# Optimization experiments

Hardware: AMD Instinct MI355X
Metric: run time of the kernel (lower is better)

Reference implementation:

```python
import jax, jax.numpy as jnp
import numpy as np

B, L, D, H = 2, 2048, 2048, 16
HD = D // H  # 128, must be even for RoPE


def rope(x, seq_len, theta=10000.0):
    """Apply RoPE to x of shape [B, H, L, Dh]."""
    d = x.shape[-1]
    freqs = 1.0 / theta ** (jnp.arange(0, d, 2, dtype=x.dtype) / d)  # [d/2]
    t = jnp.arange(seq_len, dtype=x.dtype)
    f = jnp.outer(t, freqs)                      # [L, d/2]
    sin = jnp.repeat(jnp.sin(f), 2, axis=-1)     # [L, d]
    cos = jnp.repeat(jnp.cos(f), 2, axis=-1)
    x1, x2 = x[..., ::2], x[..., 1::2]
    x_rot = jnp.stack([-x2, x1], axis=-1).reshape(x.shape)
    return x * cos + x_rot * sin


def setup_inputs() -> dict:
    key = jax.random.key(0)
    k1, k2, k3 = jax.random.split(key, 3)
    x = jax.random.normal(k1, (B, L, D), dtype=jnp.float32)
    w_qkv = jax.random.normal(k2, (D, 3 * D), dtype=jnp.float32) * (1.0 / np.sqrt(D))
    w_proj = jax.random.normal(k3, (D, D), dtype=jnp.float32) * (1.0 / np.sqrt(D))
    return {"x": x, "w_qkv": w_qkv, "w_proj": w_proj}


def reference(x, w_qkv, w_proj):
    Bc, Lc, Dc = x.shape
    scale = 1.0 / np.sqrt(HD)
    qkv = (x @ w_qkv).reshape(Bc, Lc, 3, H, HD)
    q, k, v = qkv[:, :, 0], qkv[:, :, 1], qkv[:, :, 2]   # [B, L, H, Dh]
    # transpose to [B, H, L, Dh], then RoPE (position axis = L)
    q = rope(jnp.transpose(q, (0, 2, 1, 3)), Lc)
    k = rope(jnp.transpose(k, (0, 2, 1, 3)), Lc)
    v = jnp.transpose(v, (0, 2, 1, 3))
    att = jnp.einsum("bhqd,bhkd->bhqk", q, k) * scale   # [B, H, L, L]
    att = jax.nn.softmax(att, axis=-1)
    out = jnp.einsum("bhqk,bhkd->bhqd", att, v)          # [B, H, L, Dh]
    out = jnp.transpose(out, (0, 2, 1, 3)).reshape(Bc, Lc, Dc)
    return out @ w_proj
```

## Files before the change

kernel.cpp:

```cpp
#include <hip/hip_runtime.h>
#include <hip/hip_bf16.h>
#include <cstdint>

typedef short short8 __attribute__((ext_vector_type(8)));
typedef float f32x4 __attribute__((ext_vector_type(4)));

#define AS1 __attribute__((address_space(1)))
#define AS3 __attribute__((address_space(3)))

static __device__ __forceinline__ void async_cp16(const void* g, void* l) {
  __builtin_amdgcn_global_load_lds((const AS1 unsigned int*)g, (AS3 unsigned int*)l, 16, 0, 0);
}

static __device__ __forceinline__ ushort f2bf(float f) {
  unsigned u = __builtin_bit_cast(unsigned, f);
  u += 0x7fffu + ((u >> 16) & 1u);
  return (ushort)(u >> 16);
}
static __device__ __forceinline__ float bf2f(ushort h) {
  unsigned u = ((unsigned)h) << 16;
  return __builtin_bit_cast(float, u);
}

#define FENCE asm volatile("" ::: "memory")
#define BARRIER do { FENCE; __builtin_amdgcn_s_barrier(); FENCE; } while (0)
#define WAITLGKM asm volatile("s_waitcnt lgkmcnt(0)" ::: "memory")
#define WAITVM(N) asm volatile("s_waitcnt vmcnt(" #N ")" ::: "memory")

__global__ void cvt_bf16_kernel(const float* __restrict__ in, ushort* __restrict__ out, int n4) {
  int i = blockIdx.x * blockDim.x + threadIdx.x;
  if (i >= n4) return;
  float4 v = ((const float4*)in)[i];
  ushort4 o;
  o.x = f2bf(v.x); o.y = f2bf(v.y); o.z = f2bf(v.z); o.w = f2bf(v.w);
  ((ushort4*)out)[i] = o;
}

__global__ void transpose_cvt_kernel(const float* __restrict__ in, ushort* __restrict__ out,
                                     int R, int C) {
  __shared__ ushort tile[32][33];
  int c0 = blockIdx.x * 32, r0 = blockIdx.y * 32;
  int tx = threadIdx.x, ty = threadIdx.y;
  for (int j = 0; j < 32; j += 8)
    tile[ty + j][tx] = f2bf(in[(size_t)(r0 + ty + j) * C + c0 + tx]);
  __syncthreads();
  for (int j = 0; j < 32; j += 8)
    out[(size_t)(c0 + ty + j) * R + r0 + tx] = tile[tx][ty + j];
}

__global__ __launch_bounds__(512, 2) void gemm_qkv_kernel(
    const ushort* __restrict__ A, const ushort* __restrict__ Bt,
    ushort* __restrict__ qr, ushort* __restrict__ kr, ushort* __restrict__ vt,
    int K, int N) {
  __shared__ __align__(16) ushort smem[65536];
  const int tid = threadIdx.x;
  const int wave = tid >> 6, lane = tid & 63;
  const int wm = wave >> 2, wn = wave & 3;
  const int m0 = blockIdx.y * 256, n0 = blockIdx.x * 256;
  const int frl = lane & 15, fq = lane >> 4;
  const int sx = fq ^ (frl & 7);
  const int srow = tid >> 3;
  const int slog8 = (((tid & 7) ^ ((tid >> 3) & 7)) << 3);

  const ushort* aG = A + (size_t)(m0 + srow) * K + slog8;
  const ushort* bG = Bt + (size_t)(n0 + srow) * K + slog8;
  ushort* lw = smem + wave * 512;

  f32x4 acc[8][4] = {};
  short8 aF[4][2], bF[2][2][2];

  auto stA = [&](int tt, int h) {
    ushort* l = lw + (tt & 1) * 32768 + h * 8192;
    const ushort* g = aG + (size_t)(h * 128) * K + tt * 64;
    async_cp16(g, l);
    async_cp16(g + (size_t)64 * K, l + 4096);
  };
  auto stB = [&](int tt, int h) {
    ushort* l = lw + (tt & 1) * 32768 + 16384 + h * 8192;
    const ushort* g = bG + (size_t)(h * 128) * K + tt * 64;
    async_cp16(g, l);
    async_cp16(g + (size_t)64 * K, l + 4096);
  };
  auto LDA = [&](int buf, int mh) {
#pragma unroll
    for (int mf = 0; mf < 4; ++mf)
#pragma unroll
      for (int kk = 0; kk < 2; ++kk)
        aF[mf][kk] = *(const short8*)(smem + buf * 32768 +
            (wm * 128 + mh * 64 + mf * 16 + frl) * 64 + ((sx ^ (kk << 2)) << 3));
  };
  auto LDB = [&](int buf, int nh) {
#pragma unroll
    for (int j = 0; j < 2; ++j)
#pragma unroll
      for (int kk = 0; kk < 2; ++kk)
        bF[nh][j][kk] = *(const short8*)(smem + buf * 32768 + 16384 +
            (wn * 64 + nh * 32 + j * 16 + frl) * 64 + ((sx ^ (kk << 2)) << 3));
  };
  auto MFMAQ = [&](int mh, int nh) {
    __builtin_amdgcn_s_setprio(1);
#pragma unroll
    for (int mf = 0; mf < 4; ++mf)
#pragma unroll
      for (int j = 0; j < 2; ++j)
#pragma unroll
        for (int kk = 0; kk < 2; ++kk)
          acc[mh * 4 + mf][nh * 2 + j] = __builtin_amdgcn_mfma_f32_16x16x32_bf16(
              aF[mf][kk], bF[nh][j][kk], acc[mh * 4 + mf][nh * 2 + j], 0, 0, 0);
    __builtin_amdgcn_s_setprio(0);
  };

  stB(0, 0); stB(0, 1); stA(0, 0); stA(0, 1);
  stB(1, 0); stB(1, 1);
  WAITVM(4);
  BARRIER;

  const int NT = K >> 6;
  for (int i = 0; i < NT / 2 - 1; ++i) {
    const int t = 2 * i;
    LDA(0, 0); LDB(0, 0); stA(t + 1, 0);
    BARRIER; WAITLGKM; MFMAQ(0, 0); BARRIER;
    LDB(0, 1); stA(t + 1, 1);
    BARRIER; WAITLGKM; MFMAQ(0, 1); BARRIER;
    LDA(0, 1); stB(t + 2, 0);
    BARRIER; WAITLGKM; MFMAQ(1, 0); BARRIER;
    stB(t + 2, 1);
    BARRIER; WAITLGKM; MFMAQ(1, 1); WAITVM(4); BARRIER;
    LDA(1, 0); LDB(1, 0); stA(t + 2, 0);
    BARRIER; WAITLGKM; MFMAQ(0, 0); BARRIER;
    LDB(1, 1); stA(t + 2, 1);
    BARRIER; WAITLGKM; MFMAQ(0, 1); BARRIER;
    LDA(1, 1); stB(t + 3, 0);
    BARRIER; WAITLGKM; MFMAQ(1, 0); BARRIER;
    stB(t + 3, 1);
    BARRIER; WAITLGKM; MFMAQ(1, 1); WAITVM(4); BARRIER;
  }
  {
    const int t = NT - 2;
    LDA(0, 0); LDB(0, 0); stA(t + 1, 0);
    BARRIER; WAITLGKM; MFMAQ(0, 0); BARRIER;
    LDB(0, 1); stA(t + 1, 1);
    BARRIER; WAITLGKM; MFMAQ(0, 1); BARRIER;
    LDA(0, 1);
    BARRIER; WAITLGKM; MFMAQ(1, 0); BARRIER;
    BARRIER; WAITLGKM; MFMAQ(1, 1); WAITVM(0); BARRIER;
    LDA(1, 0); LDB(1, 0);
    BARRIER; WAITLGKM; MFMAQ(0, 0); BARRIER;
    LDB(1, 1);
    BARRIER; WAITLGKM; MFMAQ(0, 1); BARRIER;
    LDA(1, 1);
    BARRIER; WAITLGKM; MFMAQ(1, 0); BARRIER;
    BARRIER; WAITLGKM; MFMAQ(1, 1); BARRIER;
  }

  const int rq = fq * 4;
  if (n0 < 4096) {
    ushort* dst = (n0 >= 2048) ? kr : qr;
#pragma unroll
    for (int mi = 0; mi < 8; ++mi)
#pragma unroll
      for (int ni = 0; ni < 4; ++ni) {
        int col = n0 + wn * 64 + ni * 16 + frl;
        int rem = col & 2047, h = rem >> 7, dh = rem & 127;
#pragma unroll
        for (int r = 0; r < 4; ++r) {
          int row = m0 + wm * 128 + mi * 16 + rq + r;
          int b = row >> 11, l = row & 2047;
          dst[((size_t)((b << 4) + h) * 2048 + l) * 128 + dh] = f2bf(acc[mi][ni][r]);
        }
      }
  } else {
    ushort* vtile = smem + wave * 1024;
    const int col0 = n0 + wn * 64;
    const int row0 = m0 + wm * 128;
    const int b = row0 >> 11, l0 = row0 & 2047;
    const int swz = (frl & 3) << 4;
#pragma unroll
    for (int hm = 0; hm < 2; ++hm)
#pragma unroll
      for (int ni = 0; ni < 4; ++ni) {
#pragma unroll
        for (int mi = 0; mi < 4; ++mi)
#pragma unroll
          for (int r = 0; r < 4; ++r) {
            int ll = mi * 16 + rq + r;
            vtile[frl * 64 + (ll ^ swz)] = f2bf(acc[hm * 4 + mi][ni][r]);
          }
#pragma unroll
        for (int tt = 0; tt < 2; ++tt) {
          int dl = tt * 8 + (lane >> 3);
          int l8 = (lane & 7) * 8;
          int lsw = l8 ^ ((dl & 3) << 4);
          int rem = (col0 + ni * 16 + dl) & 2047;
          int h = rem >> 7, dh = rem & 127;
          *(short8*)(vt + ((size_t)((b << 4) + h) * 128 + dh) * 2048 + l0 + hm * 64 + l8) =
              *(const short8*)(vtile + dl * 64 + lsw);
        }
      }
  }
}

__global__ __launch_bounds__(256) void gemm_out_kernel(
    const ushort* __restrict__ A, const ushort* __restrict__ Bt,
    float* __restrict__ C, int K, int N) {
  __shared__ __align__(16) ushort As[128 * 32];
  __shared__ __align__(16) ushort Bs[128 * 32];
  const int tid = threadIdx.x;
  const int wave = tid >> 6, lane = tid & 63;
  const int wr = (wave >> 1) * 64, wc = (wave & 1) * 64;
  const int m0 = blockIdx.y * 128, n0 = blockIdx.x * 128;
  const int l4 = lane >> 2, lb8 = (lane & 3) * 8;
  const int fr = lane & 15, fq8 = (lane >> 4) * 8;

  f32x4 acc[4][4] = {};

  for (int k0 = 0; k0 < K; k0 += 32) {
#pragma unroll
    for (int j = 0; j < 2; ++j) {
      const int r = wave * 32 + j * 16 + l4;
      async_cp16(A + (size_t)(m0 + r) * K + k0 + lb8, As + wave * 1024 + j * 512);
      async_cp16(Bt + (size_t)(n0 + r) * K + k0 + lb8, Bs + wave * 1024 + j * 512);
    }
    __syncthreads();
    short8 af[4], bf_[4];
#pragma unroll
    for (int i = 0; i < 4; ++i) {
      af[i] = *(const short8*)(As + (wr + i * 16 + fr) * 32 + fq8);
      bf_[i] = *(const short8*)(Bs + (wc + i * 16 + fr) * 32 + fq8);
    }
#pragma unroll
    for (int mi = 0; mi < 4; ++mi)
#pragma unroll
      for (int ni = 0; ni < 4; ++ni)
        acc[mi][ni] = __builtin_amdgcn_mfma_f32_16x16x32_bf16(af[mi], bf_[ni], acc[mi][ni], 0, 0, 0);
    __syncthreads();
  }

  const int rq = (lane >> 4) * 4;
#pragma unroll
  for (int mi = 0; mi < 4; ++mi)
#pragma unroll
    for (int ni = 0; ni < 4; ++ni) {
      int col = n0 + wc + ni * 16 + fr;
#pragma unroll
      for (int r = 0; r < 4; ++r) {
        int row = m0 + wr + mi * 16 + rq + r;
        C[(size_t)row * N + col] = acc[mi][ni][r];
      }
    }
}

__global__ void rope_kernel(ushort* __restrict__ q, ushort* __restrict__ k) {
  int idx = blockIdx.x * 256 + threadIdx.x;
  int i = idx & 63;
  int l = (idx >> 6) & 2047;
  int bh = idx >> 17;
  float inv = __builtin_amdgcn_exp2f(-(float)i * (13.287712379549449f / 64.0f));
  float f = (float)l * inv;
  float s, c;
  sincosf(f, &s, &c);
  size_t base = ((size_t)bh * 2048 + l) * 128 + 2 * i;
  float q0 = bf2f(q[base]), q1 = bf2f(q[base + 1]);
  q[base] = f2bf(q0 * c - q1 * s);
  q[base + 1] = f2bf(q1 * c + q0 * s);
  float k0 = bf2f(k[base]), k1 = bf2f(k[base + 1]);
  k[base] = f2bf(k0 * c - k1 * s);
  k[base + 1] = f2bf(k1 * c + k0 * s);
}

__global__ __launch_bounds__(512, 4) void flash_kernel(
    const ushort* __restrict__ qr, const ushort* __restrict__ kr,
    const ushort* __restrict__ vtg, ushort* __restrict__ att) {
  __shared__ __align__(16) ushort Ks[64 * 136];
  __shared__ __align__(16) ushort Vt[128 * 68];
  __shared__ __align__(16) ushort Ps[8 * 16 * 68];

  const int tid = threadIdx.x;
  const int wave = tid >> 6, lane = tid & 63;
  const int bid = blockIdx.x;
  const int swzb = (bid & 7) * 64 + (bid >> 3);
  const int qt = swzb & 15;
  const int bh = swzb >> 4;
  const int q0 = qt * 128 + wave * 16;
  const size_t bh_base = (size_t)bh * 2048 * 128;

  const int fr = lane & 15;
  const int fq = lane >> 4;
  const float cs = 0.08838834764831845f * 1.4426950408889634f;

  short8 qf[4];
  {
    const ushort* qp = qr + bh_base + (size_t)(q0 + fr) * 128 + fq * 8;
#pragma unroll
    for (int kc = 0; kc < 4; ++kc) qf[kc] = *(const short8*)(qp + kc * 32);
  }

  f32x4 oacc[8];
#pragma unroll
  for (int i = 0; i < 8; ++i) oacc[i] = (f32x4){0.f, 0.f, 0.f, 0.f};
  float l_r[4] = {0.f, 0.f, 0.f, 0.f};

  const int krow = tid >> 3;
  const int kc8 = tid & 7;
  const int vrow = tid >> 2;
  const int vc8 = tid & 3;

  ushort* pw = &Ps[wave * 16 * 68];

  short8 kpre[2], vpre[2];
  {
    const ushort* kg = kr + bh_base + (size_t)krow * 128;
    const ushort* vg = vtg + bh_base + (size_t)vrow * 2048;
#pragma unroll
    for (int i = 0; i < 2; ++i) {
      kpre[i] = *(const short8*)(kg + (kc8 + 8 * i) * 8);
      vpre[i] = *(const short8*)(vg + (vc8 + 4 * i) * 8);
    }
  }

  for (int kt = 0; kt < 32; ++kt) {
    __syncthreads();
#pragma unroll
    for (int i = 0; i < 2; ++i) {
      *(short8*)(&Ks[krow * 136 + (kc8 + 8 * i) * 8]) = kpre[i];
      *(short8*)(&Vt[vrow * 68 + (vc8 + 4 * i) * 8]) = vpre[i];
    }
    __syncthreads();
    if (kt < 31) {
      const ushort* kg = kr + bh_base + (size_t)((kt + 1) * 64 + krow) * 128;
      const ushort* vg = vtg + bh_base + (size_t)vrow * 2048 + (kt + 1) * 64;
#pragma unroll
      for (int i = 0; i < 2; ++i) {
        kpre[i] = *(const short8*)(kg + (kc8 + 8 * i) * 8);
        vpre[i] = *(const short8*)(vg + (vc8 + 4 * i) * 8);
      }
    }

    float sv[4][4];
    __builtin_amdgcn_s_setprio(1);
#pragma unroll
    for (int nt = 0; nt < 4; ++nt) {
      f32x4 a = (f32x4){0.f, 0.f, 0.f, 0.f};
#pragma unroll
      for (int kc = 0; kc < 4; ++kc) {
        short8 kf = *(const short8*)(&Ks[(nt * 16 + fr) * 136 + kc * 32 + fq * 8]);
        a = __builtin_amdgcn_mfma_f32_16x16x32_bf16(qf[kc], kf, a, 0, 0, 0);
      }
#pragma unroll
      for (int r = 0; r < 4; ++r) sv[nt][r] = a[r];
    }
    __builtin_amdgcn_s_setprio(0);

#pragma unroll
    for (int nt = 0; nt < 4; ++nt)
#pragma unroll
      for (int r = 0; r < 4; ++r) {
        float pv = __builtin_amdgcn_exp2f(sv[nt][r] * cs);
        l_r[r] += pv;
        pw[(fq * 4 + r) * 68 + nt * 16 + fr] = f2bf(pv);
      }

    __builtin_amdgcn_s_setprio(1);
#pragma unroll
    for (int kc2 = 0; kc2 < 2; ++kc2) {
      short8 pf = *(const short8*)(&pw[fr * 68 + kc2 * 32 + fq * 8]);
#pragma unroll
      for (int dt = 0; dt < 8; ++dt) {
        short8 vf = *(const short8*)(&Vt[(dt * 16 + fr) * 68 + kc2 * 32 + fq * 8]);
        oacc[dt] = __builtin_amdgcn_mfma_f32_16x16x32_bf16(pf, vf, oacc[dt], 0, 0, 0);
      }
    }
    __builtin_amdgcn_s_setprio(0);
  }

  const int b = bh >> 4, h = bh & 15;
#pragma unroll
  for (int r = 0; r < 4; ++r) {
    float l = l_r[r];
    l += __shfl_xor(l, 1);
    l += __shfl_xor(l, 2);
    l += __shfl_xor(l, 4);
    l += __shfl_xor(l, 8);
    float inv = 1.0f / l;
    size_t row = (size_t)(b * 2048 + q0 + fq * 4 + r) * 2048 + h * 128;
#pragma unroll
    for (int dt = 0; dt < 8; ++dt)
      att[row + dt * 16 + fr] = f2bf(oacc[dt][r] * inv);
  }
}

extern "C" void kernel_launch(void* const* d_in, const int* in_sizes, int n_in,
                              void* d_out, int out_size, void* d_ws, size_t ws_size,
                              hipStream_t stream) {
  const float* x = (const float*)d_in[0];
  const float* w_qkv = (const float*)d_in[1];
  const float* w_proj = (const float*)d_in[2];
  float* out = (float*)d_out;

  char* p = (char*)d_ws;
  ushort* xb = (ushort*)p;  p += (size_t)4096 * 2048 * 2;
  ushort* wqt = (ushort*)p; p += (size_t)6144 * 2048 * 2;
  ushort* wpt = (ushort*)p; p += (size_t)2048 * 2048 * 2;
  ushort* qr = (ushort*)p;  p += (size_t)32 * 2048 * 128 * 2;
  ushort* kr = (ushort*)p;  p += (size_t)32 * 2048 * 128 * 2;
  ushort* vt = (ushort*)p;  p += (size_t)32 * 2048 * 128 * 2;
  ushort* att = (ushort*)p; p += (size_t)4096 * 2048 * 2;

  cvt_bf16_kernel<<<8192, 256, 0, stream>>>(x, xb, 4096 * 2048 / 4);
  transpose_cvt_kernel<<<dim3(192, 64), dim3(32, 8), 0, stream>>>(w_qkv, wqt, 2048, 6144);
  transpose_cvt_kernel<<<dim3(64, 64), dim3(32, 8), 0, stream>>>(w_proj, wpt, 2048, 2048);
  gemm_qkv_kernel<<<dim3(24, 16), 512, 0, stream>>>(xb, wqt, qr, kr, vt, 2048, 6144);
  rope_kernel<<<16384, 256, 0, stream>>>(qr, kr);
  flash_kernel<<<512, 512, 0, stream>>>(qr, kr, vt, att);
  gemm_out_kernel<<<dim3(16, 32), 256, 0, stream>>>(att, wpt, out, 2048, 2048);
}
```

Baseline: 447.9 us.

## Load K and V fragments directly from global memory, dropping LDS staging

The flash attention kernel no longer stages K and V tiles through shared memory with register prefetch and two block barriers per iteration. Each wave now reads its MFMA operand fragments for K and transposed V straight from global memory, relying on L1/L2 caching to share them among the eight waves of a block. This removes the barriers and LDS traffic and frees LDS, but each wave issues its own global loads with no prefetch, so load latency is exposed and cache bandwidth pressure goes up.

```diff
diff --git a/kernel.cpp b/kernel.cpp
--- a/kernel.cpp
+++ b/kernel.cpp
@@ -271,8 +271,6 @@
 __global__ __launch_bounds__(512, 4) void flash_kernel(
     const ushort* __restrict__ qr, const ushort* __restrict__ kr,
     const ushort* __restrict__ vtg, ushort* __restrict__ att) {
-  __shared__ __align__(16) ushort Ks[64 * 136];
-  __shared__ __align__(16) ushort Vt[128 * 68];
   __shared__ __align__(16) ushort Ps[8 * 16 * 68];
 
   const int tid = threadIdx.x;
@@ -300,50 +298,21 @@
   for (int i = 0; i < 8; ++i) oacc[i] = (f32x4){0.f, 0.f, 0.f, 0.f};
   float l_r[4] = {0.f, 0.f, 0.f, 0.f};
 
-  const int krow = tid >> 3;
-  const int kc8 = tid & 7;
-  const int vrow = tid >> 2;
-  const int vc8 = tid & 3;
-
   ushort* pw = &Ps[wave * 16 * 68];
-
-  short8 kpre[2], vpre[2];
-  {
-    const ushort* kg = kr + bh_base + (size_t)krow * 128;
-    const ushort* vg = vtg + bh_base + (size_t)vrow * 2048;
-#pragma unroll
-    for (int i = 0; i < 2; ++i) {
-      kpre[i] = *(const short8*)(kg + (kc8 + 8 * i) * 8);
-      vpre[i] = *(const short8*)(vg + (vc8 + 4 * i) * 8);
-    }
-  }
-
+  const ushort* Kb = kr + bh_base + (size_t)fr * 128 + fq * 8;
+  const ushort* Vb = vtg + bh_base + (size_t)fr * 2048 + fq * 8;
+
+#pragma unroll 1
   for (int kt = 0; kt < 32; ++kt) {
-    __syncthreads();
-#pragma unroll
-    for (int i = 0; i < 2; ++i) {
-      *(short8*)(&Ks[krow * 136 + (kc8 + 8 * i) * 8]) = kpre[i];
-      *(short8*)(&Vt[vrow * 68 + (vc8 + 4 * i) * 8]) = vpre[i];
-    }
-    __syncthreads();
-    if (kt < 31) {
-      const ushort* kg = kr + bh_base + (size_t)((kt + 1) * 64 + krow) * 128;
-      const ushort* vg = vtg + bh_base + (size_t)vrow * 2048 + (kt + 1) * 64;
-#pragma unroll
-      for (int i = 0; i < 2; ++i) {
-        kpre[i] = *(const short8*)(kg + (kc8 + 8 * i) * 8);
-        vpre[i] = *(const short8*)(vg + (vc8 + 4 * i) * 8);
-      }
-    }
-
     float sv[4][4];
     __builtin_amdgcn_s_setprio(1);
 #pragma unroll
     for (int nt = 0; nt < 4; ++nt) {
+      const ushort* kp = Kb + kt * 8192 + nt * 2048;
       f32x4 a = (f32x4){0.f, 0.f, 0.f, 0.f};
 #pragma unroll
       for (int kc = 0; kc < 4; ++kc) {
-        short8 kf = *(const short8*)(&Ks[(nt * 16 + fr) * 136 + kc * 32 + fq * 8]);
+        short8 kf = *(const short8*)(kp + kc * 32);
         a = __builtin_amdgcn_mfma_f32_16x16x32_bf16(qf[kc], kf, a, 0, 0, 0);
       }
 #pragma unroll
@@ -364,9 +333,10 @@
 #pragma unroll
     for (int kc2 = 0; kc2 < 2; ++kc2) {
       short8 pf = *(const short8*)(&pw[fr * 68 + kc2 * 32 + fq * 8]);
+      const ushort* vp = Vb + kt * 64 + kc2 * 32;
 #pragma unroll
       for (int dt = 0; dt < 8; ++dt) {
-        short8 vf = *(const short8*)(&Vt[(dt * 16 + fr) * 68 + kc2 * 32 + fq * 8]);
+        short8 vf = *(const short8*)(vp + dt * 32768);
         oacc[dt] = __builtin_amdgcn_mfma_f32_16x16x32_bf16(pf, vf, oacc[dt], 0, 0, 0);
       }
     }
```

Measured after the change: 774.1 us. +72.8%, slower.
